# Optimization experiments

Hardware: AMD Instinct MI355X
Metric: run time of the kernel (lower is better)

Reference implementation:

```python
import jax, jax.numpy as jnp
import numpy as np

NUM_USER, BATCH, NUM_NT = 8, 16384, 128
T = 0.3  # SE threshold from the original module


def setup_inputs() -> dict:
    key = jax.random.key(0)
    k1, k2 = jax.random.split(key)
    h = jax.random.normal(k1, (NUM_USER, BATCH, NUM_NT), dtype=jnp.float32)
    v = jax.random.normal(k2, (NUM_USER, BATCH, NUM_NT), dtype=jnp.float32)
    N = jnp.ones((), dtype=jnp.float32)
    return {"h": h, "v": v, "N": N}


def reference(h, v, N):
    num_user, batch, num_nt = h.shape
    d = num_nt // 2
    # split real/imag halves into complex views
    h_c = jax.lax.complex(h[..., :d], h[..., d:])  # (user, batch, d)
    v_c = jax.lax.complex(v[..., :d], v[..., d:])  # (user, batch, d)
    # per-sample Frobenius norm over (user, d) and power scaling to sqrt(num_user)
    norms = jnp.sqrt(jnp.sum(jnp.real(v_c) ** 2 + jnp.imag(v_c) ** 2, axis=(0, 2)))  # (batch,)
    scale = jnp.sqrt(jnp.float32(num_user)) / norms
    v_scaled = v_c * scale[None, :, None]
    # signal: diag(h_user @ v_user^H) per sample == row-wise complex dot, with SCALED v
    S = jnp.abs(jnp.sum(h_c * jnp.conj(v_scaled), axis=-1)) ** 2  # (user, batch)
    # interference: original uses UNSCALED v[j] (faithful to source)
    A = jnp.einsum('ibt,jbt->ijb', h_c, jnp.conj(v_c))  # (user_i, user_j, batch)
    Iall = jnp.abs(A) ** 2
    Ip = jnp.sum(Iall, axis=1) - jnp.einsum('iib->ib', Iall)  # exclude j == i
    SINR = S / (Ip + N)
    R_user = jnp.log2(1.0 + SINR)  # (user, batch)
    R_per_user_p = jnp.mean(R_user, axis=1)  # (user,)
    # Rp = sum_i ( -R_user_i + 10^(T - R_user_i) ) per sample
    Rp = jnp.sum(10.0 ** (T - R_user) - R_user, axis=0)  # (batch,)
    return jnp.mean(Rp), R_per_user_p, jnp.sum(R_per_user_p)
```

## Files before the change

### kernel.cpp

```cpp
#include <hip/hip_runtime.h>


constexpr int U_    = 8;
constexpr int B_    = 16384;
constexpr int NT_   = 128;
constexpr int NBLK_ = 2048;
constexpr int WPB_  = 4;
constexpr int TW_   = NBLK_ * WPB_;
constexpr int IT_   = B_ / TW_;
constexpr int RS_   = 36;
constexpr float T_THRESH = 0.3f;
constexpr float LOG2_10  = 3.3219280948873623f;

__device__ __forceinline__ float waveReduceSum(float v) {
    #pragma unroll
    for (int m = 1; m < 64; m <<= 1) v += __shfl_xor(v, m, 64);
    return v;
}

__device__ __forceinline__ float hw_log2(float x) { return __builtin_amdgcn_logf(x); }
__device__ __forceinline__ float hw_exp2(float x) { return __builtin_amdgcn_exp2f(x); }

__global__ __launch_bounds__(256, 4) void se_main(const float* __restrict__ h,
                                                  const float* __restrict__ vv,
                                                  const float* __restrict__ Np,
                                                  float* __restrict__ partial) {
    __shared__ float lds[WPB_][2][16 * RS_];
    __shared__ float red_f[WPB_];
    __shared__ float red_R[WPB_][U_];

    const int tid  = threadIdx.x;
    const int wave = tid >> 6;
    const int lane = tid & 63;
    const int ui   = lane >> 3;
    const int uj   = lane & 7;
    const float Nval = Np[0];

    float* hb = lds[wave][0];
    float* vb = lds[wave][1];

    const int gwave = blockIdx.x * WPB_ + wave;

    const float* hrb = h  + (size_t)ui * ((size_t)B_ * NT_) + uj * 4;
    const float* vrb = vv + (size_t)ui * ((size_t)B_ * NT_) + uj * 4;

    float lane_sumR = 0.0f;
    float lane_sumf = 0.0f;

    #pragma unroll
    for (int it = 0; it < IT_; ++it) {
        const int b = gwave + it * TW_;
        float nsq = 0.0f, are = 0.0f, aim = 0.0f;

        #pragma unroll
        for (int x = 0; x < 2; ++x) {
            const int off = b * NT_ + x * 32;
            const float4 rh0 = *reinterpret_cast<const float4*>(hrb + off);
            const float4 rh1 = *reinterpret_cast<const float4*>(hrb + off + 64);
            const float4 rv0 = *reinterpret_cast<const float4*>(vrb + off);
            const float4 rv1 = *reinterpret_cast<const float4*>(vrb + off + 64);

            *reinterpret_cast<float4*>(&hb[(2 * ui + 0) * RS_ + uj * 4]) = rh0;
            *reinterpret_cast<float4*>(&hb[(2 * ui + 1) * RS_ + uj * 4]) = rh1;
            *reinterpret_cast<float4*>(&vb[(2 * ui + 0) * RS_ + uj * 4]) = rv0;
            *reinterpret_cast<float4*>(&vb[(2 * ui + 1) * RS_ + uj * 4]) = rv1;
            nsq += rv0.x * rv0.x + rv0.y * rv0.y + rv0.z * rv0.z + rv0.w * rv0.w
                 + rv1.x * rv1.x + rv1.y * rv1.y + rv1.z * rv1.z + rv1.w * rv1.w;

            const float* hre = &hb[(2 * ui) * RS_];
            const float* him = hre + RS_;
            const float* vre = &vb[(2 * uj) * RS_];
            const float* vim = vre + RS_;
            #pragma unroll
            for (int ks = 0; ks < 32; ks += 4) {
                const float4 hr = *reinterpret_cast<const float4*>(hre + ks);
                const float4 hi = *reinterpret_cast<const float4*>(him + ks);
                const float4 vr = *reinterpret_cast<const float4*>(vre + ks);
                const float4 vi = *reinterpret_cast<const float4*>(vim + ks);
                are += hr.x * vr.x + hi.x * vi.x;
                aim += hi.x * vr.x - hr.x * vi.x;
                are += hr.y * vr.y + hi.y * vi.y;
                aim += hi.y * vr.y - hr.y * vi.y;
                are += hr.z * vr.z + hi.z * vi.z;
                aim += hi.z * vr.z - hr.z * vi.z;
                are += hr.w * vr.w + hi.w * vi.w;
                aim += hi.w * vr.w - hr.w * vi.w;
            }
        }

        const float normsq = waveReduceSum(nsq);
        const float Iall = are * are + aim * aim;

        const float diag = __shfl(Iall, ui * 9, 64);
        float rowsum = Iall;
        rowsum += __shfl_xor(rowsum, 1, 64);
        rowsum += __shfl_xor(rowsum, 2, 64);
        rowsum += __shfl_xor(rowsum, 4, 64);

        const float Ip   = rowsum - diag;
        const float S    = (8.0f / normsq) * diag;
        const float SINR = S / (Ip + Nval);
        const float R    = hw_log2(1.0f + SINR);

        lane_sumR += R;
        lane_sumf += hw_exp2((T_THRESH - R) * LOG2_10) - R;
    }

    const float wf = waveReduceSum(lane_sumf) * 0.125f;
    if (lane == 0) red_f[wave] = wf;
    if (uj == 0)   red_R[wave][ui] = lane_sumR;
    __syncthreads();

    if (tid < U_) {
        float s = 0.0f;
        #pragma unroll
        for (int w = 0; w < WPB_; ++w) s += red_R[w][tid];
        partial[blockIdx.x * 9 + 1 + tid] = s;
    } else if (tid == U_) {
        float s = 0.0f;
        #pragma unroll
        for (int w = 0; w < WPB_; ++w) s += red_f[w];
        partial[blockIdx.x * 9] = s;
    }
}

__global__ __launch_bounds__(1024) void se_final(const float* __restrict__ partial,
                                                 float* __restrict__ out) {
    __shared__ float acc[16][9];
    const int tid = threadIdx.x, w = tid >> 6, l = tid & 63;

    float v[9];
    #pragma unroll
    for (int s = 0; s < 9; ++s)
        v[s] = partial[tid * 9 + s] + partial[(tid + 1024) * 9 + s];

    #pragma unroll
    for (int s = 0; s < 9; ++s) {
        float t = v[s];
        #pragma unroll
        for (int m = 1; m < 64; m <<= 1) t += __shfl_xor(t, m, 64);
        if (l == 0) acc[w][s] = t;
    }
    __syncthreads();

    if (tid == 0) {
        float sums[9];
        #pragma unroll
        for (int s = 0; s < 9; ++s) {
            float t = acc[0][s];
            #pragma unroll
            for (int ww = 1; ww < 16; ++ww) t += acc[ww][s];
            sums[s] = t;
        }
        const float inv = 1.0f / (float)B_;
        out[0] = sums[0] * inv;
        float tot = 0.0f;
        #pragma unroll
        for (int i = 0; i < U_; ++i) {
            const float r = sums[1 + i] * inv;
            out[1 + i] = r;
            tot += r;
        }
        out[9] = tot;
    }
}

extern "C" void kernel_launch(void* const* d_in, const int* in_sizes, int n_in,
                              void* d_out, int out_size, void* d_ws, size_t ws_size,
                              hipStream_t stream) {
    const float* h  = (const float*)d_in[0];
    const float* v  = (const float*)d_in[1];
    const float* Np = (const float*)d_in[2];
    float* out      = (float*)d_out;
    float* partial  = (float*)d_ws;

    se_main<<<NBLK_, 256, 0, stream>>>(h, v, Np, partial);
    se_final<<<1, 1024, 0, stream>>>(partial, out);
}
```

Before: 156.4 us.

## Double-buffer global loads directly into LDS with swizzled layout

Replaces register-staged global loads followed by LDS stores with direct global-to-LDS loads (global_load_lds), double-buffered so the next phase's tile is fetched while the current one is computed. The LDS tile uses a rotation swizzle in place of the padded row stride, avoiding bank conflicts without padding. It relies on manual s_waitcnt vmcnt counting and sched barriers, which are fragile if the compiler emits other vector-memory ops. There is also no explicit wave-level barrier between the asynchronous LDS writes and the reads.

```diff
diff --git a/kernel.cpp b/kernel.cpp
--- a/kernel.cpp
+++ b/kernel.cpp
@@ -8,9 +8,16 @@
 constexpr int WPB_  = 4;
 constexpr int TW_   = NBLK_ * WPB_;
 constexpr int IT_   = B_ / TW_;
-constexpr int RS_   = 36;
+constexpr size_t UST_ = (size_t)B_ * NT_;
 constexpr float T_THRESH = 0.3f;
 constexpr float LOG2_10  = 3.3219280948873623f;
+
+typedef __attribute__((address_space(3))) void lds_void;
+typedef const __attribute__((address_space(1))) void g_void;
+
+__device__ __forceinline__ void gload16(const float* g, float* l) {
+    __builtin_amdgcn_global_load_lds((g_void*)g, (lds_void*)l, 16, 0, 0);
+}
 
 __device__ __forceinline__ float waveReduceSum(float v) {
     #pragma unroll
@@ -25,7 +32,7 @@
                                                   const float* __restrict__ vv,
                                                   const float* __restrict__ Np,
                                                   float* __restrict__ partial) {
-    __shared__ float lds[WPB_][2][16 * RS_];
+    __shared__ __align__(16) float lds[WPB_][2][2][512];
     __shared__ float red_f[WPB_];
     __shared__ float red_R[WPB_][U_];
 
@@ -36,47 +43,67 @@
     const int uj   = lane & 7;
     const float Nval = Np[0];
 
-    float* hb = lds[wave][0];
-    float* vb = lds[wave][1];
-
     const int gwave = blockIdx.x * WPB_ + wave;
 
-    const float* hrb = h  + (size_t)ui * ((size_t)B_ * NT_) + uj * 4;
-    const float* vrb = vv + (size_t)ui * ((size_t)B_ * NT_) + uj * 4;
+    const int u0 = lane >> 4;
+    const int p_ = (lane >> 3) & 1;
+    const int s_ = lane & 7;
+    const int g0 = (s_ - u0) & 7;
+    const int g1 = (s_ - (u0 + 4)) & 7;
+    const size_t off0 = (size_t)u0 * UST_ + (size_t)(p_ * 64 + g0 * 4);
+    const size_t off1 = (size_t)(u0 + 4) * UST_ + (size_t)(p_ * 64 + g1 * 4);
+    const float* h0 = h  + off0;  const float* h1 = h  + off1;
+    const float* v0 = vv + off0;  const float* v1 = vv + off1;
+
+    float (*T0)[512] = lds[wave][0];
+    float (*T1)[512] = lds[wave][1];
 
     float lane_sumR = 0.0f;
     float lane_sumf = 0.0f;
 
+    {
+        const size_t po = (size_t)gwave * NT_;
+        gload16(h0 + po, &T0[0][0]);   gload16(h1 + po, &T0[0][256]);
+        gload16(v0 + po, &T0[1][0]);   gload16(v1 + po, &T0[1][256]);
+    }
+
     #pragma unroll
     for (int it = 0; it < IT_; ++it) {
-        const int b = gwave + it * TW_;
         float nsq = 0.0f, are = 0.0f, aim = 0.0f;
-
         #pragma unroll
         for (int x = 0; x < 2; ++x) {
-            const int off = b * NT_ + x * 32;
-            const float4 rh0 = *reinterpret_cast<const float4*>(hrb + off);
-            const float4 rh1 = *reinterpret_cast<const float4*>(hrb + off + 64);
-            const float4 rv0 = *reinterpret_cast<const float4*>(vrb + off);
-            const float4 rv1 = *reinterpret_cast<const float4*>(vrb + off + 64);
-
-            *reinterpret_cast<float4*>(&hb[(2 * ui + 0) * RS_ + uj * 4]) = rh0;
-            *reinterpret_cast<float4*>(&hb[(2 * ui + 1) * RS_ + uj * 4]) = rh1;
-            *reinterpret_cast<float4*>(&vb[(2 * ui + 0) * RS_ + uj * 4]) = rv0;
-            *reinterpret_cast<float4*>(&vb[(2 * ui + 1) * RS_ + uj * 4]) = rv1;
+            const int ph = it * 2 + x;
+            float (*TC)[512] = (ph & 1) ? T1 : T0;
+            float (*TN)[512] = (ph & 1) ? T0 : T1;
+
+            if (ph < 2 * IT_ - 1) {
+                const int bn = gwave + ((ph + 1) >> 1) * TW_;
+                const int xn = (ph + 1) & 1;
+                const size_t po = (size_t)bn * NT_ + (size_t)(xn * 32);
+                gload16(h0 + po, &TN[0][0]);   gload16(h1 + po, &TN[0][256]);
+                gload16(v0 + po, &TN[1][0]);   gload16(v1 + po, &TN[1][256]);
+                asm volatile("s_waitcnt vmcnt(4)" ::: "memory");
+            } else {
+                asm volatile("s_waitcnt vmcnt(0)" ::: "memory");
+            }
+            __builtin_amdgcn_sched_barrier(0);
+
+            const float* vrow = &TC[1][ui * 64];
+            const float4 rv0 = *reinterpret_cast<const float4*>(vrow + ((uj + ui) & 7) * 4);
+            const float4 rv1 = *reinterpret_cast<const float4*>(vrow + 32 + ((uj + ui) & 7) * 4);
             nsq += rv0.x * rv0.x + rv0.y * rv0.y + rv0.z * rv0.z + rv0.w * rv0.w
                  + rv1.x * rv1.x + rv1.y * rv1.y + rv1.z * rv1.z + rv1.w * rv1.w;
 
-            const float* hre = &hb[(2 * ui) * RS_];
-            const float* him = hre + RS_;
-            const float* vre = &vb[(2 * uj) * RS_];
-            const float* vim = vre + RS_;
+            const float* ha = &TC[0][ui * 64];
+            const float* va = &TC[1][uj * 64];
             #pragma unroll
-            for (int ks = 0; ks < 32; ks += 4) {
-                const float4 hr = *reinterpret_cast<const float4*>(hre + ks);
-                const float4 hi = *reinterpret_cast<const float4*>(him + ks);
-                const float4 vr = *reinterpret_cast<const float4*>(vre + ks);
-                const float4 vi = *reinterpret_cast<const float4*>(vim + ks);
+            for (int c = 0; c < 8; ++c) {
+                const int hs = ((c + ui) & 7) * 4;
+                const int vs = ((c + uj) & 7) * 4;
+                const float4 hr = *reinterpret_cast<const float4*>(ha + hs);
+                const float4 hi = *reinterpret_cast<const float4*>(ha + 32 + hs);
+                const float4 vr = *reinterpret_cast<const float4*>(va + vs);
+                const float4 vi = *reinterpret_cast<const float4*>(va + 32 + vs);
                 are += hr.x * vr.x + hi.x * vi.x;
                 aim += hi.x * vr.x - hr.x * vi.x;
                 are += hr.y * vr.y + hi.y * vi.y;
```

After: 157.2 us. Within noise of the previous version (+0.5%).
